# Kernel tuning notes

Hardware: AMD Instinct MI355X
Metric: run time of the kernel (lower is better)

Reference implementation:

```python
import jax, jax.numpy as jnp
import numpy as np
from jax import lax

EPS = 1e-5

def quantize_ternary(w):
    # scale = mean(|w|).clamp_min(1e-5) computed on detached weight
    scale = jnp.maximum(jnp.mean(jnp.abs(lax.stop_gradient(w))), EPS)
    ws = w / scale
    # STE: forward uses round+clamp, backward is identity in ws
    wq = lax.stop_gradient(jnp.clip(jnp.round(ws), -1.0, 1.0) - ws) + ws
    return wq * scale

def conv2d(x, w, b):
    # x: [N,C,H,W], w: [O,I,kh,kw], stride 1, pad 1 -> same spatial size
    out = lax.conv_general_dilated(
        x, w, window_strides=(1, 1), padding=[(1, 1), (1, 1)],
        dimension_numbers=("NCHW", "OIHW", "NCHW"))
    return out + b[None, :, None, None]

def setup_inputs() -> dict:
    key = jax.random.key(0)
    k1, k2, k3, k4, k5 = jax.random.split(key, 5)
    N, C_in, C_out, H, W, K = 16, 64, 64, 128, 128, 3
    fan_in = C_in * K * K
    bound = 1.0 / np.sqrt(fan_in)
    x = jax.random.normal(k1, (N, C_in, H, W), dtype=jnp.float32)
    w = jax.random.uniform(k2, (C_out, C_in, K, K), minval=-bound, maxval=bound, dtype=jnp.float32)
    b = jax.random.uniform(k3, (C_out,), minval=-bound, maxval=bound, dtype=jnp.float32)
    # growth child: kaiming-uniform-like init scaled by 0.01, zero bias
    w_child = jax.random.uniform(k4, (C_out, C_in, K, K), minval=-bound, maxval=bound, dtype=jnp.float32) * 0.01
    b_child = jnp.zeros((C_out,), dtype=jnp.float32)
    gate = jnp.zeros((1,), dtype=jnp.float32)  # growth_gate buffer
    return {"x": x, "w": w, "b": b, "w_child": w_child, "b_child": b_child, "gate": gate}

def reference(x, w, b, w_child, b_child, gate):
    out = conv2d(x, quantize_ternary(w), b)
    child_out = conv2d(x, quantize_ternary(w_child), b_child)
    g = jax.nn.sigmoid(gate)  # shape [1], broadcasts
    return out + g * child_out
```

## Files before the change

### kernel.cpp

```cpp
#include <hip/hip_runtime.h>
#include <math.h>


typedef __attribute__((ext_vector_type(8))) short short8;
typedef __attribute__((ext_vector_type(4))) float float4v;

__device__ inline unsigned short f2bf(float f) {
  union { float f; unsigned u; } v; v.f = f;
  unsigned u = v.u;
  return (unsigned short)((u + 0x7FFFu + ((u >> 16) & 1u)) >> 16);
}

__global__ __launch_bounds__(1024) void reduce_abs_part(const float* __restrict__ w,
                                                        const float* __restrict__ wc,
                                                        double* __restrict__ part) {
  const int base = blockIdx.x * 4096 + threadIdx.x;
  double a = 0.0, c = 0.0;
#pragma unroll
  for (int i = 0; i < 4; ++i) {
    a += (double)fabsf(w[base + i * 1024]);
    c += (double)fabsf(wc[base + i * 1024]);
  }
#pragma unroll
  for (int off = 32; off > 0; off >>= 1) {
    a += __shfl_down(a, off);
    c += __shfl_down(c, off);
  }
  __shared__ double sa[16], sc[16];
  int wv = threadIdx.x >> 6;
  if ((threadIdx.x & 63) == 0) { sa[wv] = a; sc[wv] = c; }
  __syncthreads();
  if (threadIdx.x == 0) {
    double ta = 0.0, tc = 0.0;
#pragma unroll
    for (int i = 0; i < 16; ++i) { ta += sa[i]; tc += sc[i]; }
    part[blockIdx.x] = ta;
    part[9 + blockIdx.x] = tc;
  }
}

__global__ void quant_combine(const float* __restrict__ w, const float* __restrict__ wc,
                              const float* __restrict__ b, const float* __restrict__ bc,
                              const float* __restrict__ gate, const double* __restrict__ part,
                              unsigned short* __restrict__ wq, float* __restrict__ beff) {
  double s0 = 0.0, s1 = 0.0;
#pragma unroll
  for (int i = 0; i < 9; ++i) { s0 += part[i]; s1 += part[9 + i]; }
  const float sw = fmaxf((float)(s0 * (1.0 / 36864.0)), 1e-5f);
  const float sc = fmaxf((float)(s1 * (1.0 / 36864.0)), 1e-5f);
  const float g = 1.0f / (1.0f + expf(-gate[0]));
  int idx = blockIdx.x * 256 + threadIdx.x;
  int tap = idx >> 12;
  int oc = (idx >> 6) & 63;
  int ci = idx & 63;
  int src = oc * 576 + ci * 9 + tap;
  float q1 = fminf(1.f, fmaxf(-1.f, rintf(w[src] / sw))) * sw;
  float q2 = fminf(1.f, fmaxf(-1.f, rintf(wc[src] / sc))) * sc;
  wq[idx] = f2bf(q1 + g * q2);
  if (idx < 64) beff[idx] = b[idx] + g * bc[idx];
}

__global__ __launch_bounds__(256) void transpose_x(const float* __restrict__ x,
                                                   unsigned short* __restrict__ xp) {
  const int bid = blockIdx.x;
  const int n = bid / 130;
  const int hp = bid - n * 130;
  unsigned short* dst = xp + (size_t)(n * 130 + hp) * (130 * 64);
  const int tid = threadIdx.x;

  if (hp == 0 || hp == 129) {
    for (int j = tid; j < 1040; j += 256) ((short8*)dst)[j] = (short8)0;
    return;
  }
  const int h = hp - 1;
  __shared__ unsigned tile[128 * 33];

  const float* src = x + (size_t)n * 64 * 16384 + h * 128;
  for (int k = tid; k < 4096; k += 256) {
    int ci2 = k >> 7;
    int c = k & 127;
    unsigned lo = f2bf(src[(2 * ci2) * 16384 + c]);
    unsigned hi = f2bf(src[(2 * ci2 + 1) * 16384 + c]);
    tile[c * 33 + ci2] = lo | (hi << 16);
  }
  if (tid < 8) ((short8*)dst)[tid] = (short8)0;
  else if (tid < 16) ((short8*)dst)[1032 + (tid - 8)] = (short8)0;
  __syncthreads();
  for (int j = tid; j < 1024; j += 256) {
    int c = j >> 3;
    int q = j & 7;
    const unsigned* tp = &tile[c * 33 + q * 4];
    unsigned u0 = tp[0], u1 = tp[1], u2 = tp[2], u3 = tp[3];
    short8 v;
    v[0] = (short)(u0 & 0xffff); v[1] = (short)(u0 >> 16);
    v[2] = (short)(u1 & 0xffff); v[3] = (short)(u1 >> 16);
    v[4] = (short)(u2 & 0xffff); v[5] = (short)(u2 >> 16);
    v[6] = (short)(u3 & 0xffff); v[7] = (short)(u3 >> 16);
    ((short8*)dst)[8 + j] = v;
  }
}

__global__ __launch_bounds__(256, 2) void conv_mfma(
    const unsigned short* __restrict__ xp, const unsigned short* __restrict__ wq,
    const float* __restrict__ beff, float* __restrict__ out) {
  extern __shared__ __align__(16) char smem[];
  const int bid = blockIdx.x;
  const int xcd = bid & 7;
  const int u = bid >> 3;
  const int n = xcd * 2 + (u >> 6);
  const int h0 = (u & 63) * 2;
  const int tid = threadIdx.x;
  const int lane = tid & 63;
  const int wv = tid >> 6;
  const int rw = wv >> 1;
  const int pxh = (wv & 1) * 64;
  const int ln15 = lane & 15;
  const int lq = lane >> 4;
  const int koff = lq << 3;

  const unsigned short* slab = xp + (size_t)(n * 130 + h0) * (130 * 64);
  for (int j = tid; j < 4160; j += 256) {
    int r = j / 1040;
    int rem = j - r * 1040;
    int p = rem >> 3;
    int q = rem & 7;
    short8 v = *(const short8*)(slab + j * 8);
    *(short8*)(smem + ((r * 1040 + (p << 3) + (q ^ (p & 7))) << 4)) = v;
  }
  __syncthreads();

  const unsigned short* wbase = wq + ln15 * 64 + koff;

  short8 A[2][2][4], B[2][2][4];
  float4v acc[4][4] = {};

  auto load_tap = [&](int tap, short8 Ab[2][4], short8 Bb[2][4]) {
    const int dh = tap / 3;
    const int dw = tap - dh * 3;
    const int r = rw + dh;
    const int pb = pxh + ln15 + dw;
    const int swz = lq ^ (pb & 7);
    const int b0 = ((r * 130 + pb) << 7) + (swz << 4);
    const unsigned short* wp = wbase + tap * 4096;
#pragma unroll
    for (int mf = 0; mf < 4; ++mf) {
      Ab[0][mf] = *(const short8*)(smem + (b0 + mf * 2048));
      Ab[1][mf] = *(const short8*)(smem + ((b0 ^ 64) + mf * 2048));
    }
#pragma unroll
    for (int qd = 0; qd < 4; ++qd) {
      Bb[0][qd] = *(const short8*)(wp + qd * 1024);
      Bb[1][qd] = *(const short8*)(wp + qd * 1024 + 32);
    }
  };

  load_tap(0, A[0], B[0]);
#pragma unroll
  for (int tap = 0; tap < 9; ++tap) {
    const int cur = tap & 1, nxt = cur ^ 1;
    if (tap < 8) load_tap(tap + 1, A[nxt], B[nxt]);
    __builtin_amdgcn_s_setprio(1);
#pragma unroll
    for (int cc2 = 0; cc2 < 2; ++cc2)
#pragma unroll
      for (int mf = 0; mf < 4; ++mf)
#pragma unroll
        for (int qd = 0; qd < 4; ++qd)
          acc[mf][qd] = __builtin_amdgcn_mfma_f32_16x16x32_bf16(
              A[cur][cc2][mf], B[cur][cc2][qd], acc[mf][qd], 0, 0, 0);
    __builtin_amdgcn_s_setprio(0);
  }

  const int rq = lane >> 4;
  float bias[4];
#pragma unroll
  for (int q = 0; q < 4; ++q) bias[q] = beff[q * 16 + ln15];
#pragma unroll
  for (int mf = 0; mf < 4; ++mf) {
#pragma unroll
    for (int qd = 0; qd < 4; ++qd) {
      float4v v = acc[mf][qd] + bias[qd];
      int oc = qd * 16 + ln15;
      float* op = out + (((n * 64 + oc) * 128 + h0 + rw) * 128 + pxh + mf * 16 + rq * 4);
      *(float4v*)op = v;
    }
  }
}

extern "C" void kernel_launch(void* const* d_in, const int* in_sizes, int n_in,
                              void* d_out, int out_size, void* d_ws, size_t ws_size,
                              hipStream_t stream) {
  const float* x = (const float*)d_in[0];
  const float* w = (const float*)d_in[1];
  const float* b = (const float*)d_in[2];
  const float* wc = (const float*)d_in[3];
  const float* bc = (const float*)d_in[4];
  const float* gate = (const float*)d_in[5];

  unsigned short* wq = (unsigned short*)d_ws;
  float* beff = (float*)((char*)d_ws + 73728);
  double* part = (double*)((char*)d_ws + 73984);
  unsigned short* xp = (unsigned short*)((char*)d_ws + 74240);

  transpose_x<<<16 * 130, 256, 0, stream>>>(x, xp);
  reduce_abs_part<<<9, 1024, 0, stream>>>(w, wc, part);
  quant_combine<<<144, 256, 0, stream>>>(w, wc, b, bc, gate, part, wq, beff);
  conv_mfma<<<16 * 64, 256, 66560, stream>>>(xp, wq, beff, (float*)d_out);
}
```

Before: 174.1 us.

## Fuse input NCHW-to-NHWC bf16 transpose into the conv kernel's LDS staging

Removes the separate transpose_x kernel and its padded bf16 intermediate buffer. Each conv block now reads the four fp32 input rows (including the halo rows) directly from NCHW global memory, converts them to bf16, and writes them into swizzled shared memory, zeroing the padding columns and out-of-range rows. This drops a kernel launch and a full write and read of the intermediate tensor. In exchange, each input row is read as fp32 by two blocks because of halo overlap, and every block does its own conversion.

```diff
diff --git a/kernel.cpp b/kernel.cpp
--- a/kernel.cpp
+++ b/kernel.cpp
@@ -60,48 +60,8 @@
   if (idx < 64) beff[idx] = b[idx] + g * bc[idx];
 }
 
-__global__ __launch_bounds__(256) void transpose_x(const float* __restrict__ x,
-                                                   unsigned short* __restrict__ xp) {
-  const int bid = blockIdx.x;
-  const int n = bid / 130;
-  const int hp = bid - n * 130;
-  unsigned short* dst = xp + (size_t)(n * 130 + hp) * (130 * 64);
-  const int tid = threadIdx.x;
-
-  if (hp == 0 || hp == 129) {
-    for (int j = tid; j < 1040; j += 256) ((short8*)dst)[j] = (short8)0;
-    return;
-  }
-  const int h = hp - 1;
-  __shared__ unsigned tile[128 * 33];
-
-  const float* src = x + (size_t)n * 64 * 16384 + h * 128;
-  for (int k = tid; k < 4096; k += 256) {
-    int ci2 = k >> 7;
-    int c = k & 127;
-    unsigned lo = f2bf(src[(2 * ci2) * 16384 + c]);
-    unsigned hi = f2bf(src[(2 * ci2 + 1) * 16384 + c]);
-    tile[c * 33 + ci2] = lo | (hi << 16);
-  }
-  if (tid < 8) ((short8*)dst)[tid] = (short8)0;
-  else if (tid < 16) ((short8*)dst)[1032 + (tid - 8)] = (short8)0;
-  __syncthreads();
-  for (int j = tid; j < 1024; j += 256) {
-    int c = j >> 3;
-    int q = j & 7;
-    const unsigned* tp = &tile[c * 33 + q * 4];
-    unsigned u0 = tp[0], u1 = tp[1], u2 = tp[2], u3 = tp[3];
-    short8 v;
-    v[0] = (short)(u0 & 0xffff); v[1] = (short)(u0 >> 16);
-    v[2] = (short)(u1 & 0xffff); v[3] = (short)(u1 >> 16);
-    v[4] = (short)(u2 & 0xffff); v[5] = (short)(u2 >> 16);
-    v[6] = (short)(u3 & 0xffff); v[7] = (short)(u3 >> 16);
-    ((short8*)dst)[8 + j] = v;
-  }
-}
-
-__global__ __launch_bounds__(256, 2) void conv_mfma(
-    const unsigned short* __restrict__ xp, const unsigned short* __restrict__ wq,
+__global__ __launch_bounds__(256, 2) void conv_fused(
+    const float* __restrict__ x, const unsigned short* __restrict__ wq,
     const float* __restrict__ beff, float* __restrict__ out) {
   extern __shared__ __align__(16) char smem[];
   const int bid = blockIdx.x;
@@ -118,14 +78,38 @@
   const int lq = lane >> 4;
   const int koff = lq << 3;
 
-  const unsigned short* slab = xp + (size_t)(n * 130 + h0) * (130 * 64);
-  for (int j = tid; j < 4160; j += 256) {
-    int r = j / 1040;
-    int rem = j - r * 1040;
-    int p = rem >> 3;
-    int q = rem & 7;
-    short8 v = *(const short8*)(slab + j * 8);
-    *(short8*)(smem + ((r * 1040 + (p << 3) + (q ^ (p & 7))) << 4)) = v;
+  const float* xn = x + (size_t)n * (64 * 16384);
+
+  if (tid < 64) {
+    int r = tid >> 4;
+    int q = (tid >> 1) & 7;
+    int px = (tid & 1) * 129;
+    int swz = q ^ (px & 7);
+    *(short8*)(smem + ((r * 1040 + px * 8 + swz) << 4)) = (short8)0;
+  }
+
+  const int w128 = tid & 127;
+  const int hi = tid >> 7;
+#pragma unroll 4
+  for (int pass = 0; pass < 16; ++pass) {
+    const int c2 = pass * 2 + hi;
+    const int r = c2 >> 3;
+    const int q = c2 & 7;
+    const int h = h0 + r - 1;
+    short8 v = (short8)0;
+    if ((unsigned)h < 128u) {
+      const float* sp = xn + q * 8 * 16384 + h * 128 + w128;
+      float f0 = sp[0 * 16384], f1 = sp[1 * 16384], f2 = sp[2 * 16384],
+            f3 = sp[3 * 16384], f4 = sp[4 * 16384], f5 = sp[5 * 16384],
+            f6 = sp[6 * 16384], f7 = sp[7 * 16384];
+      v[0] = (short)f2bf(f0); v[1] = (short)f2bf(f1);
+      v[2] = (short)f2bf(f2); v[3] = (short)f2bf(f3);
+      v[4] = (short)f2bf(f4); v[5] = (short)f2bf(f5);
+      v[6] = (short)f2bf(f6); v[7] = (short)f2bf(f7);
+    }
+    const int px = w128 + 1;
+    const int swz = q ^ (px & 7);
+    *(short8*)(smem + ((r * 1040 + px * 8 + swz) << 4)) = v;
   }
   __syncthreads();
 
@@ -200,10 +184,8 @@
   unsigned short* wq = (unsigned short*)d_ws;
   float* beff = (float*)((char*)d_ws + 73728);
   double* part = (double*)((char*)d_ws + 73984);
-  unsigned short* xp = (unsigned short*)((char*)d_ws + 74240);
 
-  transpose_x<<<16 * 130, 256, 0, stream>>>(x, xp);
   reduce_abs_part<<<9, 1024, 0, stream>>>(w, wc, part);
   quant_combine<<<144, 256, 0, stream>>>(w, wc, b, bc, gate, part, wq, beff);
-  conv_mfma<<<16 * 64, 256, 66560, stream>>>(xp, wq, beff, (float*)d_out);
+  conv_fused<<<16 * 64, 256, 66560, stream>>>(x, wq, beff, (float*)d_out);
 }
```

Measured after the change: 165.8 us. -4.8%, faster.
